# Kernel optimization log

Hardware: AMD Instinct MI355X
Metric: run time of the kernel (lower is better)

## Reference

```python
import jax, jax.numpy as jnp
import numpy as np

LOG2PI = float(np.log(2.0 * np.pi))
VAR = 1e-4
LOGVAR = float(np.log(VAR))


def _gauss_lp(x, mean, dim):
    # MVN log_prob with covariance VAR * I_dim
    sq = jnp.sum((x - mean) ** 2, axis=-1)
    return -0.5 * (dim * (LOG2PI + LOGVAR) + sq / VAR)


def setup_inputs() -> dict:
    B, T, D, H, K = 32, 512, 256, 512, 8
    key = jax.random.key(0)
    ks = jax.random.split(key, 20)
    s = 0.05
    return {
        "x_input": jax.random.normal(ks[0], (B, T, D), jnp.float32),
        "y_train": jax.random.normal(ks[1], (B, T, D), jnp.float32),
        "sampled_h": jax.random.normal(ks[2], (B, T, H), jnp.float32),
        "initials": jax.random.normal(ks[3], (K,), jnp.float32),
        # per-state single-layer RNNs (tanh), weights [K,H,D]/[K,H,H]
        "Wih": jax.random.normal(ks[4], (K, H, D), jnp.float32) * s,
        "Whh": jax.random.normal(ks[5], (K, H, H), jnp.float32) * s,
        "bih": jax.random.normal(ks[6], (K, H), jnp.float32) * s,
        "bhh": jax.random.normal(ks[7], (K, H), jnp.float32) * s,
        # transition RNNCell (h0=0, so only input path + both biases matter)
        "Wt_ih": jax.random.normal(ks[8], (K * K, H), jnp.float32) * s,
        "bt": jax.random.normal(ks[9], (K * K,), jnp.float32) * s,
        # Emission MLP H -> 32 -> 64 -> D
        "W1": jax.random.normal(ks[10], (32, H), jnp.float32) * s,
        "b1": jax.random.normal(ks[11], (32,), jnp.float32) * s,
        "W2": jax.random.normal(ks[12], (64, 32), jnp.float32) * s,
        "b2": jax.random.normal(ks[13], (64,), jnp.float32) * s,
        "W3": jax.random.normal(ks[14], (D, 64), jnp.float32) * s,
        "b3": jax.random.normal(ks[15], (D,), jnp.float32) * s,
    }


def reference(x_input, y_train, sampled_h, initials, Wih, Whh, bih, bhh,
              Wt_ih, bt, W1, b1, W2, b2, W3, b3):
    B, T, D = x_input.shape
    H = sampled_h.shape[-1]
    K = initials.shape[0]
    lse = jax.scipy.special.logsumexp

    # initial log-probs (same for every batch row)
    prob_initial = jnp.broadcast_to(initials - lse(initials), (B, K))

    # ---- prob_all_h: per-state RNN step log-likelihoods ----
    h_prev = sampled_h[:, :-1]  # [B,T-1,H]
    pre = (jnp.einsum('btd,khd->btkh', x_input[:, 1:], Wih)
           + jnp.einsum('bth,kgh->btkg', h_prev, Whh)
           + bih[None, None] + bhh[None, None])  # [B,T-1,K,H]
    x_out = jnp.tanh(pre)
    lp_rest = _gauss_lp(sampled_h[:, 1:, None, :], x_out, H)  # [B,T-1,K]
    lp0 = -0.5 * H * (LOG2PI + LOGVAR)  # log_prob of the mean itself at t=0
    prob_all_h = jnp.concatenate(
        [jnp.full((B, 1, K), lp0, jnp.float32), lp_rest], axis=1)  # [B,T,K]

    # ---- prob_all_s: transition log-probs (normalized over axis=2) ----
    trans = jnp.tanh(jnp.einsum('bth,ch->btc', h_prev, Wt_ih) + bt)
    trans = trans.reshape(B, T - 1, K, K)
    s_rest = trans - lse(trans, axis=2, keepdims=True)
    s0 = jnp.broadcast_to(jnp.eye(K, dtype=jnp.float32), (B, 1, K, K))
    prob_all_s = jnp.concatenate([s0, s_rest], axis=1)  # [B,T,K,K]

    # ---- prob_all_y: emission MLP + MVN log-prob ----
    h1 = jax.nn.relu(sampled_h @ W1.T + b1)
    h2 = jax.nn.relu(h1 @ W2.T + b2)
    em = h2 @ W3.T + b3  # [B,T,D]
    prob_all_y = _gauss_lp(y_train, em, D)  # [B,T]

    log_e = prob_all_h + prob_all_y[..., None]  # [B,T,K]

    # ---- forward pass (Baum-Welch alpha, log-space) ----
    s_tm = jnp.swapaxes(prob_all_s[:, 1:], 0, 1)  # [T-1,B,K,K]
    e_tm = jnp.swapaxes(log_e[:, 1:], 0, 1)       # [T-1,B,K]
    alpha0 = prob_initial + log_e[:, 0]

    def fstep(a, xs):
        s_t, e_t = xs
        a_new = e_t + lse(a[:, None, :] + s_t, axis=2)  # s[b,i,j]=logp(i|j)
        return a_new, a_new

    _, alphas = jax.lax.scan(fstep, alpha0, (s_tm, e_tm))
    forward_prob = jnp.concatenate(
        [alpha0[:, None], jnp.swapaxes(alphas, 0, 1)], axis=1)  # [B,T,K]

    # ---- backward pass (beta) ----
    betaT = jnp.zeros((B, K), jnp.float32)

    def bstep(b, xs):
        s_t1, e_t1 = xs
        b_new = lse(s_t1 + (e_t1 + b)[:, :, None], axis=1)
        return b_new, b_new

    _, betas = jax.lax.scan(bstep, betaT, (s_tm, e_tm), reverse=True)
    backward_prob = jnp.concatenate(
        [jnp.swapaxes(betas, 0, 1), betaT[:, None]], axis=1)  # [B,T,K]

    # ---- gammas ----
    ab = forward_prob + backward_prob
    gamma1 = ab - lse(ab, axis=2, keepdims=True)  # [B,T,K]
    pair = (forward_prob[:, :-1, None, :] + prob_all_s[:, 1:]
            + (log_e[:, 1:] + backward_prob[:, 1:])[:, :, :, None])
    gamma2 = pair - lse(pair, axis=(2, 3), keepdims=True)  # [B,T-1,K,K]

    return (prob_initial, prob_all_s, prob_all_h, prob_all_y,
            gamma1, gamma2, forward_prob, backward_prob)
```

## Files before the change

kernel.cpp:

```cpp
#include <hip/hip_runtime.h>

typedef _Float16 f16;
typedef _Float16 f16x8 __attribute__((ext_vector_type(8)));
typedef float f32x16 __attribute__((ext_vector_type(16)));

#define NB 32
#define NT 512
#define ND 256
#define NH 512
#define M_REAL 16352
#define RDIM 768
#define TILE_ELEMS 98304
#define NTN 33

#define OFF_PI 0
#define OFF_S  256
#define OFF_H  1048832
#define OFF_Y  1179904
#define OFF_G1 1196288
#define OFF_G2 1327360
#define OFF_F  2373888
#define OFF_BW 2504960

#define WS_A    0
#define WS_B    25165824
#define WS_BIAS 31653888
#define WS_SQ   31671296
#define WS_NEED 33768448

#define CH_CONST 1887.3506062251f
#define CY_CONST 943.6753031126f
#define LOG2E 1.4426950408889634f
#define LN2 0.6931471805599453f

#define CA_BLOCKS 1024
#define CB_BLOCKS 264
#define EM_BASE   1288
#define CONV_GRID 2312

__device__ __forceinline__ float fexp2(float x) { return __builtin_amdgcn_exp2f(x); }
__device__ __forceinline__ float flog2(float x) { return __builtin_amdgcn_logf(x); }
__device__ __forceinline__ float ftanh(float x) {
    x = fminf(10.f, fmaxf(-10.f, x));
    float t = fexp2(x * 2.885390081777927f);
    return (t - 1.f) * __builtin_amdgcn_rcpf(t + 1.f);
}
__device__ __forceinline__ float lse8v(const float* z) {
    float M = fmaxf(fmaxf(fmaxf(z[0], z[1]), fmaxf(z[2], z[3])),
                    fmaxf(fmaxf(z[4], z[5]), fmaxf(z[6], z[7])));
    const float e0 = fexp2((z[0] - M) * LOG2E), e1 = fexp2((z[1] - M) * LOG2E);
    const float e2 = fexp2((z[2] - M) * LOG2E), e3 = fexp2((z[3] - M) * LOG2E);
    const float e4 = fexp2((z[4] - M) * LOG2E), e5 = fexp2((z[5] - M) * LOG2E);
    const float e6 = fexp2((z[6] - M) * LOG2E), e7 = fexp2((z[7] - M) * LOG2E);
    const float s = ((e0 + e1) + (e2 + e3)) + ((e4 + e5) + (e6 + e7));
    return M + LN2 * flog2(s);
}

__global__ __launch_bounds__(256) void conv_kernel(
    const float* __restrict__ x, const float* __restrict__ h, const float* __restrict__ y,
    const float* __restrict__ Wih, const float* __restrict__ Whh,
    const float* __restrict__ bih, const float* __restrict__ bhh,
    const float* __restrict__ Wt, const float* __restrict__ btv,
    const float* __restrict__ W1, const float* __restrict__ b1,
    const float* __restrict__ W2, const float* __restrict__ b2,
    const float* __restrict__ W3, const float* __restrict__ b3, f16* __restrict__ A,
    f16* __restrict__ Bm, float* __restrict__ biasc, float* __restrict__ out) {
    __shared__ __align__(16) float smem[11904];
    const int tid = threadIdx.x;
    if (blockIdx.x < CA_BLOCKS) {
        const int m0 = blockIdx.x * 16;
        f16x8* tb = (f16x8*)smem;
#pragma unroll
        for (int i = 0; i < 6; ++i) {
            const int idx = tid + 256 * i;
            const int ml = idx / 96;
            const int ch = idx - ml * 96;
            const int m = m0 + ml;
            f16x8 pk = (f16x8)(f16)0.f;
            if (m < M_REAL) {
                const int b = m / 511;
                const int t = m - b * 511;
                const int c0 = ch * 8;
                const float* src = (c0 < ND) ? x + (size_t)(b * NT + t + 1) * ND + c0
                                             : h + (size_t)(b * NT + t) * NH + (c0 - ND);
                const float4 u = ((const float4*)src)[0];
                const float4 v = ((const float4*)src)[1];
                pk[0] = (f16)u.x; pk[1] = (f16)u.y; pk[2] = (f16)u.z; pk[3] = (f16)u.w;
                pk[4] = (f16)v.x; pk[5] = (f16)v.y; pk[6] = (f16)v.z; pk[7] = (f16)v.w;
            }
            tb[ml * 97 + ch] = pk;
        }
        __syncthreads();
        const size_t tbase = (size_t)(m0 >> 7) * TILE_ELEMS + (size_t)(m0 & 127) * 8;
#pragma unroll
        for (int i = 0; i < 6; ++i) {
            const int idx = tid + 256 * i;
            const int ch2 = idx >> 4;
            const int m2 = idx & 15;
            *(f16x8*)(A + tbase + (size_t)ch2 * 1024 + (size_t)m2 * 8) = tb[m2 * 97 + ch2];
        }
    } else if (blockIdx.x < EM_BASE) {
        const int n0 = (blockIdx.x - CA_BLOCKS) * 16;
        f16x8* tb = (f16x8*)smem;
#pragma unroll
        for (int i = 0; i < 6; ++i) {
            const int idx = tid + 256 * i;
            const int nl = idx / 96;
            const int ch = idx - nl * 96;
            const int n = n0 + nl;
            const int c0 = ch * 8;
            f16x8 pk = (f16x8)(f16)0.f;
            const float* src = nullptr;
            if (n < 4096) {
                src = (c0 < ND) ? Wih + (size_t)n * ND + c0 : Whh + (size_t)n * NH + (c0 - ND);
            } else {
                const int c = n - 4096;
                if (c < 64 && c0 >= ND) src = Wt + (size_t)c * NH + (c0 - ND);
            }
            if (src) {
                const float4 u = ((const float4*)src)[0];
                const float4 v = ((const float4*)src)[1];
                pk[0] = (f16)u.x; pk[1] = (f16)u.y; pk[2] = (f16)u.z; pk[3] = (f16)u.w;
                pk[4] = (f16)v.x; pk[5] = (f16)v.y; pk[6] = (f16)v.z; pk[7] = (f16)v.w;
            }
            tb[nl * 97 + ch] = pk;
        }
        if (tid < 16) {
            const int n = n0 + tid;
            biasc[n] = (n < 4096) ? bih[n] + bhh[n] : ((n - 4096) < 64 ? btv[n - 4096] : 0.f);
        }
        __syncthreads();
        const size_t tbase = (size_t)(n0 >> 7) * TILE_ELEMS + (size_t)(n0 & 127) * 8;
#pragma unroll
        for (int i = 0; i < 6; ++i) {
            const int idx = tid + 256 * i;
            const int ch2 = idx >> 4;
            const int m2 = idx & 15;
            *(f16x8*)(Bm + tbase + (size_t)ch2 * 1024 + (size_t)m2 * 8) = tb[m2 * 97 + ch2];
        }
    } else {
        float* ssh = smem;
        float* W2sh = smem + 8192;
        float* h1sh = smem + 10304;
        float* h2sh = smem + 10816;
        float* red = smem + 11840;
        const int wv = tid >> 6;
        const int o = tid >> 3, seg = tid & 7;
        const int p0 = (blockIdx.x - EM_BASE) * 16;
        float4 w1r[16], w3r[16];
        {
            const float4* w1p = (const float4*)(W1 + (size_t)o * NH + seg * 64);
#pragma unroll
            for (int j = 0; j < 16; ++j) w1r[j] = w1p[(j + seg * 2) & 15];
            const float4* w3p = (const float4*)(W3 + (size_t)tid * 64);
#pragma unroll
            for (int j = 0; j < 16; ++j) w3r[j] = w3p[j];
        }
        if (tid < 64) {
            for (int j = 0; j < 32; ++j) W2sh[tid * 33 + j] = W2[tid * 32 + j];
        }
        float yv[16];
#pragma unroll
        for (int pp = 0; pp < 16; ++pp) yv[pp] = y[(size_t)(p0 + pp) * ND + tid];
        const float b1r = b1[o];
        const float b2r = b2[tid & 63];
        const float b3r = b3[tid];
#pragma unroll
        for (int pp = 0; pp < 16; ++pp) {
            const float2 hv = ((const float2*)(h + (size_t)(p0 + pp) * NH))[tid];
            ssh[pp * 512 + tid * 2] = hv.x;
            ssh[pp * 512 + tid * 2 + 1] = hv.y;
        }
        __syncthreads();
#pragma unroll
        for (int pp = 0; pp < 16; ++pp) {
            const float4* s4 = (const float4*)&ssh[pp * 512 + seg * 64];
            float p = 0.f;
#pragma unroll
            for (int it = 0; it < 16; ++it) {
                const float4 sv = s4[(it + seg * 2) & 15];
                const float4 w = w1r[it];
                p += w.x * sv.x + w.y * sv.y + w.z * sv.z + w.w * sv.w;
            }
            p += __shfl_xor(p, 1, 64);
            p += __shfl_xor(p, 2, 64);
            p += __shfl_xor(p, 4, 64);
            if (seg == 0) h1sh[pp * 32 + o] = fmaxf(p + b1r, 0.f);
        }
        __syncthreads();
        {
            const int o2 = tid & 63;
#pragma unroll
            for (int it = 0; it < 4; ++it) {
                const int pp = wv * 4 + it;
                float s = b2r;
#pragma unroll
                for (int j = 0; j < 32; ++j) s += W2sh[o2 * 33 + j] * h1sh[pp * 32 + j];
                h2sh[pp * 64 + o2] = fmaxf(s, 0.f);
            }
        }
        __syncthreads();
#pragma unroll
        for (int pp = 0; pp < 16; ++pp) {
            float s = b3r;
            const float4* h24 = (const float4*)&h2sh[pp * 64];
#pragma unroll
            for (int j = 0; j < 16; ++j) {
                const float4 w = w3r[j], hb = h24[j];
                s += w.x * hb.x + w.y * hb.y + w.z * hb.z + w.w * hb.w;
            }
            const float d = yv[pp] - s;
            float sq = d * d;
#pragma unroll
            for (int off = 32; off > 0; off >>= 1) sq += __shfl_xor(sq, off, 64);
            if ((tid & 63) == 0) red[pp * 4 + wv] = sq;
        }
        __syncthreads();
        if (tid < 16) {
            out[OFF_Y + p0 + tid] =
                CY_CONST - 5000.f * (red[tid * 4] + red[tid * 4 + 1] + red[tid * 4 + 2] +
                                     red[tid * 4 + 3]);
        }
    }
}

__global__ __launch_bounds__(256) void gemm_kernel(const f16* __restrict__ A,
                                                   const f16* __restrict__ Bm,
                                                   const float* __restrict__ biasc,
                                                   const float* __restrict__ sampled_h,
                                                   float* __restrict__ sq_part,
                                                   float* __restrict__ Ps) {
    __shared__ __align__(16) f16 Ash[8 * 128 * 8];
    __shared__ __align__(16) f16 Bsh[8 * 128 * 8];
    const int tid = threadIdx.x;
    const int lane = tid & 63;
    const int wave = tid >> 6;
    const int xcd = blockIdx.x & 7;
    const int slot = blockIdx.x >> 3;
    const int tm = xcd * 16 + (slot & 15);
    const int tn = slot >> 4;
    const int m0 = tm * 128, n0 = tn * 128;
    const int l31 = lane & 31, hk = lane >> 5;

    f32x16 acc[4];
#pragma unroll
    for (int a = 0; a < 4; ++a) acc[a] = (f32x16)0.f;

    for (int kk = 0; kk < RDIM; kk += 64) {
        __syncthreads();
        const size_t abase = (size_t)tm * TILE_ELEMS + (size_t)kk * 128;
        const size_t bbase = (size_t)tn * TILE_ELEMS + (size_t)kk * 128;
#pragma unroll
        for (int inst = 0; inst < 4; ++inst) {
            const int fb = inst * 256 + wave * 64;
            const f16* ga = A + abase + (size_t)(fb + lane) * 8;
            const f16* gb = Bm + bbase + (size_t)(fb + lane) * 8;
            __builtin_amdgcn_global_load_lds(
                (const __attribute__((address_space(1))) void*)ga,
                (__attribute__((address_space(3))) void*)&Ash[fb * 8], 16, 0, 0);
            __builtin_amdgcn_global_load_lds(
                (const __attribute__((address_space(1))) void*)gb,
                (__attribute__((address_space(3))) void*)&Bsh[fb * 8], 16, 0, 0);
        }
        __syncthreads();
#pragma unroll
        for (int kc = 0; kc < 4; ++kc) {
            const int ch = kc * 2 + hk;
            const f16x8 af = *(const f16x8*)&Ash[(ch * 128 + wave * 32 + l31) * 8];
            f16x8 bfr[4];
#pragma unroll
            for (int ni = 0; ni < 4; ++ni)
                bfr[ni] = *(const f16x8*)&Bsh[(ch * 128 + ni * 32 + l31) * 8];
#pragma unroll
            for (int ni = 0; ni < 4; ++ni)
                acc[ni] = __builtin_amdgcn_mfma_f32_32x32x16_f16(af, bfr[ni], acc[ni], 0, 0, 0);
        }
    }

    if (tn == 32) {
        const float bt0 = biasc[4096 + l31];
        const float bt1 = biasc[4096 + 32 + l31];
#pragma unroll
        for (int r = 0; r < 16; ++r) {
            const int mg = m0 + wave * 32 + (r & 3) + 8 * (r >> 2) + 4 * hk;
            if (mg < M_REAL) {
                const float v0 = ftanh(acc[0][r] + bt0);
                const float v1 = ftanh(acc[1][r] + bt1);
                float M = fmaxf(v0, v1);
                M = fmaxf(M, __shfl_xor(M, 8, 64));
                M = fmaxf(M, __shfl_xor(M, 16, 64));
                float s = fexp2((v0 - M) * LOG2E) + fexp2((v1 - M) * LOG2E);
                s += __shfl_xor(s, 8, 64);
                s += __shfl_xor(s, 16, 64);
                const float lse = M + LN2 * flog2(s);
                const int b = mg / 511, t = mg - b * 511;
                const size_t base = (size_t)(b * NT + t + 1) * 64;
                Ps[base + l31] = v0 - lse;
                Ps[base + 32 + l31] = v1 - lse;
            }
        }
    } else {
        const int k0 = n0 >> 9;
        const int slot4 = (n0 >> 7) & 3;
        const float b0 = biasc[n0 + l31];
        const float b1v = biasc[n0 + 32 + l31];
        const float b2v = biasc[n0 + 64 + l31];
        const float b3v = biasc[n0 + 96 + l31];
#pragma unroll
        for (int r = 0; r < 16; ++r) {
            const int mg = m0 + wave * 32 + (r & 3) + 8 * (r >> 2) + 4 * hk;
            if (mg < M_REAL) {
                const int bb = mg / 511;
                const int tt = mg - bb * 511;
                const float* tgt = sampled_h + (size_t)((bb << 9) + tt + 1) * NH;
                const float d0 = tgt[(n0 + l31) & 511] - ftanh(acc[0][r] + b0);
                const float d1 = tgt[(n0 + 32 + l31) & 511] - ftanh(acc[1][r] + b1v);
                const float d2 = tgt[(n0 + 64 + l31) & 511] - ftanh(acc[2][r] + b2v);
                const float d3 = tgt[(n0 + 96 + l31) & 511] - ftanh(acc[3][r] + b3v);
                float rs = d0 * d0 + d1 * d1 + d2 * d2 + d3 * d3;
                rs += __shfl_xor(rs, 1, 64);
                rs += __shfl_xor(rs, 2, 64);
                rs += __shfl_xor(rs, 4, 64);
                rs += __shfl_xor(rs, 8, 64);
                rs += __shfl_xor(rs, 16, 64);
                if (l31 == 0) sq_part[(size_t)(mg * 8 + k0) * 4 + slot4] = rs;
            }
        }
    }
}

__global__ void post_kernel(const float* __restrict__ sq_part,
                            const float* __restrict__ initials, float* __restrict__ out) {
    const int g = blockIdx.x * 256 + threadIdx.x;
    const int b = g >> 12;
    const int t = (g >> 3) & 511;
    const int k = g & 7;
    float val;
    if (t == 0) {
        val = CH_CONST;
    } else {
        const int m = b * 511 + (t - 1);
        const float4 a = *(const float4*)&sq_part[(size_t)(m * 8 + k) * 4];
        val = CH_CONST - 5000.f * (a.x + a.y + a.z + a.w);
    }
    out[OFF_H + g] = val;
    if (g < 2048) {
        const int sb = g >> 6, c = g & 63;
        out[OFF_S + (size_t)sb * NT * 64 + c] = ((c >> 3) == (c & 7)) ? 1.f : 0.f;
    }
    if (g < 256) {
        float z[8];
#pragma unroll
        for (int j = 0; j < 8; ++j) z[j] = initials[j];
        out[OFF_PI + g] = z[g & 7] - lse8v(z);
    }
}

__global__ __launch_bounds__(256) void scan_kernel(const float* __restrict__ initials,
                                                   float* __restrict__ out) {
    const float* Ps = out + OFF_S;
    const float* Ph = out + OFF_H;
    const float* Py = out + OFF_Y;
    const int lane = threadIdx.x & 63;
    const int wave = threadIdx.x >> 6;
    const int b = wave * 8 + (lane >> 3);
    const int i = lane & 7;
    const int lbase = lane & ~7;

    if (blockIdx.x == 0) {
        float z0[8];
#pragma unroll
        for (int j = 0; j < 8; ++j) z0[j] = initials[j];
        float* Fw = out + OFF_F;
        float a = (z0[i] - lse8v(z0)) + CH_CONST + Py[b * NT];
        Fw[(size_t)(b * NT) * 8 + i] = a;
        float4 cA[8], cB[8]; float cH[8], cY[8];
        float4 nA[8], nB[8]; float nH[8], nY[8];
#define FLOAD(CC, A_, B_, H_, Y_)                                                  \
        _Pragma("unroll") for (int j = 0; j < 8; ++j) {                            \
            int t = 1 + (CC) * 8 + j;                                              \
            t = t > 511 ? 511 : t;                                                 \
            const size_t p = (size_t)(b * NT + t) * 64 + i * 8;                    \
            A_[j] = *(const float4*)&Ps[p];                                        \
            B_[j] = *(const float4*)&Ps[p + 4];                                    \
            H_[j] = Ph[(size_t)(b * NT + t) * 8 + i];                              \
            Y_[j] = Py[b * NT + t];                                                \
        }
#define FSTEP(CC, A_, B_, H_, Y_)                                                  \
        _Pragma("unroll") for (int j = 0; j < 8; ++j) {                            \
            const int t = 1 + (CC) * 8 + j;                                        \
            if (t < NT) {                                                          \
                float z[8];                                                        \
                z[0] = __shfl(a, lbase + 0, 64) + A_[j].x;                         \
                z[1] = __shfl(a, lbase + 1, 64) + A_[j].y;                         \
                z[2] = __shfl(a, lbase + 2, 64) + A_[j].z;                         \
                z[3] = __shfl(a, lbase + 3, 64) + A_[j].w;                         \
                z[4] = __shfl(a, lbase + 4, 64) + B_[j].x;                         \
                z[5] = __shfl(a, lbase + 5, 64) + B_[j].y;                         \
                z[6] = __shfl(a, lbase + 6, 64) + B_[j].z;                         \
                z[7] = __shfl(a, lbase + 7, 64) + B_[j].w;                         \
                a = (H_[j] + Y_[j]) + lse8v(z);                                    \
                Fw[(size_t)(b * NT + t) * 8 + i] = a;                              \
            }                                                                      \
        }
        FLOAD(0, cA, cB, cH, cY);
        for (int c = 0; c < 64; c += 2) {
            const int c1 = c + 1;
            const int c2 = (c + 2 < 64) ? c + 2 : 63;
            FLOAD(c1, nA, nB, nH, nY);
            FSTEP(c, cA, cB, cH, cY);
            FLOAD(c2, cA, cB, cH, cY);
            FSTEP(c1, nA, nB, nH, nY);
        }
#undef FLOAD
#undef FSTEP
    } else {
        float* Bw = out + OFF_BW;
        float bv = 0.f;
        Bw[(size_t)(b * NT + NT - 1) * 8 + i] = 0.f;
        float cS[8][8], nS[8][8]; float cH[8], cY[8], nH[8], nY[8];
#define BLOAD(CC, S_, H_, Y_)                                                      \
        _Pragma("unroll") for (int j = 0; j < 8; ++j) {                            \
            int t = 510 - ((CC) * 8 + j);                                          \
            t = t < 0 ? 0 : t;                                                     \
            const size_t t1 = (size_t)(b * NT + t + 1);                            \
            _Pragma("unroll") for (int ii = 0; ii < 8; ++ii)                       \
                S_[j][ii] = Ps[t1 * 64 + ii * 8 + i];                              \
            H_[j] = Ph[t1 * 8 + i];                                                \
            Y_[j] = Py[t1];                                                        \
        }
#define BSTEP(CC, S_, H_, Y_)                                                      \
        _Pragma("unroll") for (int j = 0; j < 8; ++j) {                            \
            const int t = 510 - ((CC) * 8 + j);                                    \
            if (t >= 0) {                                                          \
                const float v = H_[j] + Y_[j] + bv;                                \
                float z[8];                                                        \
                _Pragma("unroll") for (int ii = 0; ii < 8; ++ii)                   \
                    z[ii] = __shfl(v, lbase + ii, 64) + S_[j][ii];                 \
                bv = lse8v(z);                                                     \
                Bw[(size_t)(b * NT + t) * 8 + i] = bv;                             \
            }                                                                      \
        }
        BLOAD(0, cS, cH, cY);
        for (int c = 0; c < 64; c += 2) {
            const int c1 = c + 1;
            const int c2 = (c + 2 < 64) ? c + 2 : 63;
            BLOAD(c1, nS, nH, nY);
            BSTEP(c, cS, cH, cY);
            BLOAD(c2, cS, cH, cY);
            BSTEP(c1, nS, nH, nY);
        }
#undef BLOAD
#undef BSTEP
    }
}

__global__ void gamma_kernel(float* __restrict__ out) {
    const float* Ps = out + OFF_S;
    const float* Ph = out + OFF_H;
    const float* Py = out + OFF_Y;
    const float* Fw = out + OFF_F;
    const float* Bw = out + OFF_BW;
    if (blockIdx.x < 511) {
        const int gidx = blockIdx.x * 256 + threadIdx.x;
        const int pos = gidx >> 3;
        const int i = gidx & 7;
        const int b = pos / 511, t = pos - b * 511;
        const size_t t1 = (size_t)(b * NT + t + 1);
        const float ei = Ph[t1 * 8 + i] + Py[t1] + Bw[t1 * 8 + i];
        const float4 sa = ((const float4*)&Ps[(t1 * 8 + i) * 8])[0];
        const float4 sb = ((const float4*)&Ps[(t1 * 8 + i) * 8])[1];
        const float4 fa = ((const float4*)&Fw[(size_t)(b * NT + t) * 8])[0];
        const float4 fb = ((const float4*)&Fw[(size_t)(b * NT + t) * 8])[1];
        float z[8] = {fa.x + sa.x + ei, fa.y + sa.y + ei, fa.z + sa.z + ei, fa.w + sa.w + ei,
                      fb.x + sb.x + ei, fb.y + sb.y + ei, fb.z + sb.z + ei, fb.w + sb.w + ei};
        float M = fmaxf(fmaxf(fmaxf(z[0], z[1]), fmaxf(z[2], z[3])),
                        fmaxf(fmaxf(z[4], z[5]), fmaxf(z[6], z[7])));
        M = fmaxf(M, __shfl_xor(M, 1, 64));
        M = fmaxf(M, __shfl_xor(M, 2, 64));
        M = fmaxf(M, __shfl_xor(M, 4, 64));
        float s = 0.f;
#pragma unroll
        for (int j = 0; j < 8; ++j) s += fexp2((z[j] - M) * LOG2E);
        s += __shfl_xor(s, 1, 64);
        s += __shfl_xor(s, 2, 64);
        s += __shfl_xor(s, 4, 64);
        const float l = M + LN2 * flog2(s);
        float* G2 = out + OFF_G2;
        float4 o0 = {z[0] - l, z[1] - l, z[2] - l, z[3] - l};
        float4 o1 = {z[4] - l, z[5] - l, z[6] - l, z[7] - l};
        ((float4*)&G2[(size_t)gidx * 8])[0] = o0;
        ((float4*)&G2[(size_t)gidx * 8])[1] = o1;
    } else {
        const int pos = (blockIdx.x - 511) * 256 + threadIdx.x;
        const float4 fa = ((const float4*)&Fw[(size_t)pos * 8])[0];
        const float4 fb = ((const float4*)&Fw[(size_t)pos * 8])[1];
        const float4 ba = ((const float4*)&Bw[(size_t)pos * 8])[0];
        const float4 bb = ((const float4*)&Bw[(size_t)pos * 8])[1];
        float ab[8] = {fa.x + ba.x, fa.y + ba.y, fa.z + ba.z, fa.w + ba.w,
                       fb.x + bb.x, fb.y + bb.y, fb.z + bb.z, fb.w + bb.w};
        const float l = lse8v(ab);
        float* G1 = out + OFF_G1;
        float4 o0 = {ab[0] - l, ab[1] - l, ab[2] - l, ab[3] - l};
        float4 o1 = {ab[4] - l, ab[5] - l, ab[6] - l, ab[7] - l};
        ((float4*)&G1[(size_t)pos * 8])[0] = o0;
        ((float4*)&G1[(size_t)pos * 8])[1] = o1;
    }
}

extern "C" void kernel_launch(void* const* d_in, const int* in_sizes, int n_in, void* d_out,
                              int out_size, void* d_ws, size_t ws_size, hipStream_t stream) {
    const float* x = (const float*)d_in[0];
    const float* y = (const float*)d_in[1];
    const float* h = (const float*)d_in[2];
    const float* initials = (const float*)d_in[3];
    const float* Wih = (const float*)d_in[4];
    const float* Whh = (const float*)d_in[5];
    const float* bih = (const float*)d_in[6];
    const float* bhh = (const float*)d_in[7];
    const float* Wt = (const float*)d_in[8];
    const float* btv = (const float*)d_in[9];
    const float* W1 = (const float*)d_in[10];
    const float* b1 = (const float*)d_in[11];
    const float* W2 = (const float*)d_in[12];
    const float* b2 = (const float*)d_in[13];
    const float* W3 = (const float*)d_in[14];
    const float* b3 = (const float*)d_in[15];
    float* out = (float*)d_out;
    char* ws = (char*)d_ws;
    if (ws_size < (size_t)WS_NEED) return;
    f16* Aws = (f16*)(ws + WS_A);
    f16* Bws = (f16*)(ws + WS_B);
    float* biasc = (float*)(ws + WS_BIAS);
    float* sqp = (float*)(ws + WS_SQ);

    conv_kernel<<<CONV_GRID, 256, 0, stream>>>(x, h, y, Wih, Whh, bih, bhh, Wt, btv, W1, b1,
                                               W2, b2, W3, b3, Aws, Bws, biasc, out);
    gemm_kernel<<<4224, 256, 0, stream>>>(Aws, Bws, biasc, h, sqp, out + OFF_S);
    post_kernel<<<512, 256, 0, stream>>>(sqp, initials, out);
    scan_kernel<<<2, 256, 0, stream>>>(initials, out);
    gamma_kernel<<<575, 256, 0, stream>>>(out);
}
```

Measured before the change: 462.0 us.

## Parallelize HMM forward/backward scans via chunked log-semiring transfer matrices

```diff
diff --git a/kernel.cpp b/kernel.cpp
--- a/kernel.cpp
+++ b/kernel.cpp
@@ -26,12 +26,14 @@
 #define WS_B    25165824
 #define WS_BIAS 31653888
 #define WS_SQ   31671296
-#define WS_NEED 33768448
+#define WS_M    33768448
+#define WS_NEED 34292736
 
 #define CH_CONST 1887.3506062251f
 #define CY_CONST 943.6753031126f
 #define LOG2E 1.4426950408889634f
 #define LN2 0.6931471805599453f
+#define NEGINF -1e30f
 
 #define CA_BLOCKS 1024
 #define CB_BLOCKS 264
@@ -237,8 +239,8 @@
     const int wave = tid >> 6;
     const int xcd = blockIdx.x & 7;
     const int slot = blockIdx.x >> 3;
-    const int tm = xcd * 16 + (slot & 15);
-    const int tn = slot >> 4;
+    const int tm = xcd * 16 + slot / NTN;
+    const int tn = slot % NTN;
     const int m0 = tm * 128, n0 = tn * 128;
     const int l31 = lane & 31, hk = lane >> 5;
 
@@ -356,102 +358,185 @@
     }
 }
 
-__global__ __launch_bounds__(256) void scan_kernel(const float* __restrict__ initials,
-                                                   float* __restrict__ out) {
+
+template <bool WRITE>
+__device__ __forceinline__ float fwd_run(const float* __restrict__ Ps,
+                                         const float* __restrict__ Ph,
+                                         const float* __restrict__ Py,
+                                         float* __restrict__ Fw, int b, int t0,
+                                         int t1, float a, int lane) {
+    const int i = lane & 7;
+    const int base = lane & ~7;
+    float4 cA[8], cB[8], nA[8], nB[8];
+    float cH[8], cY[8], nH[8], nY[8];
+#define FLOADR(G, A_, B_, H_, Y_)                                              \
+    _Pragma("unroll") for (int jj = 0; jj < 8; ++jj) {                         \
+        int t = t0 + (G) * 8 + jj;                                             \
+        t = t > t1 ? t1 : t;                                                   \
+        const size_t p = (size_t)(b * NT + t) * 64 + i * 8;                    \
+        A_[jj] = *(const float4*)&Ps[p];                                       \
+        B_[jj] = *(const float4*)&Ps[p + 4];                                   \
+        H_[jj] = Ph[(size_t)(b * NT + t) * 8 + i];                             \
+        Y_[jj] = Py[b * NT + t];                                               \
+    }
+#define FSTEPR(G, A_, B_, H_, Y_)                                              \
+    _Pragma("unroll") for (int jj = 0; jj < 8; ++jj) {                         \
+        const int t = t0 + (G) * 8 + jj;                                       \
+        if (t <= t1) {                                                         \
+            float z[8];                                                        \
+            z[0] = __shfl(a, base + 0, 64) + A_[jj].x;                         \
+            z[1] = __shfl(a, base + 1, 64) + A_[jj].y;                         \
+            z[2] = __shfl(a, base + 2, 64) + A_[jj].z;                         \
+            z[3] = __shfl(a, base + 3, 64) + A_[jj].w;                         \
+            z[4] = __shfl(a, base + 4, 64) + B_[jj].x;                         \
+            z[5] = __shfl(a, base + 5, 64) + B_[jj].y;                         \
+            z[6] = __shfl(a, base + 6, 64) + B_[jj].z;                         \
+            z[7] = __shfl(a, base + 7, 64) + B_[jj].w;                         \
+            a = (H_[jj] + Y_[jj]) + lse8v(z);                                  \
+            if (WRITE && lane < 8) Fw[(size_t)(b * NT + t) * 8 + i] = a;       \
+        }                                                                      \
+    }
+    FLOADR(0, cA, cB, cH, cY);
+    FLOADR(1, nA, nB, nH, nY);
+    FSTEPR(0, cA, cB, cH, cY);
+    FLOADR(2, cA, cB, cH, cY);
+    FSTEPR(1, nA, nB, nH, nY);
+    FLOADR(3, nA, nB, nH, nY);
+    FSTEPR(2, cA, cB, cH, cY);
+    FSTEPR(3, nA, nB, nH, nY);
+#undef FLOADR
+#undef FSTEPR
+    return a;
+}
+
+template <bool WRITE>
+__device__ __forceinline__ float bwd_run(const float* __restrict__ Ps,
+                                         const float* __restrict__ Ph,
+                                         const float* __restrict__ Py,
+                                         float* __restrict__ Bw, int b, int tt0,
+                                         int tt1, float a, int lane) {
+    const int i = lane & 7;
+    const int base = lane & ~7;
+    float cS[8][8], nS[8][8], cH[8], cY[8], nH[8], nY[8];
+#define BLOADR(G, S_, H_, Y_)                                                  \
+    _Pragma("unroll") for (int jj = 0; jj < 8; ++jj) {                         \
+        int t = tt0 - (G) * 8 - jj;                                            \
+        t = t < tt1 ? tt1 : t;                                                 \
+        const size_t q = (size_t)(b * NT + t + 1);                             \
+        _Pragma("unroll") for (int ii = 0; ii < 8; ++ii)                       \
+            S_[jj][ii] = Ps[q * 64 + ii * 8 + i];                              \
+        H_[jj] = Ph[q * 8 + i];                                                \
+        Y_[jj] = Py[q];                                                       \
+    }
+#define BSTEPR(G, S_, H_, Y_)                                                  \
+    _Pragma("unroll") for (int jj = 0; jj < 8; ++jj) {                         \
+        const int t = tt0 - (G) * 8 - jj;                                      \
+        if (t >= tt1) {                                                        \
+            const float v = H_[jj] + Y_[jj] + a;                               \
+            float z[8];                                                        \
+            _Pragma("unroll") for (int ii = 0; ii < 8; ++ii)                   \
+                z[ii] = __shfl(v, base + ii, 64) + S_[jj][ii];                 \
+            a = lse8v(z);                                                      \
+            if (WRITE && lane < 8) Bw[(size_t)(b * NT + t) * 8 + i] = a;       \
+        }                                                                      \
+    }
+    BLOADR(0, cS, cH, cY);
+    BLOADR(1, nS, nH, nY);
+    BSTEPR(0, cS, cH, cY);
+    BLOADR(2, cS, cH, cY);
+    BSTEPR(1, nS, nH, nY);
+    BLOADR(3, nS, nH, nY);
+    BSTEPR(2, cS, cH, cY);
+    BSTEPR(3, nS, nH, nY);
+#undef BLOADR
+#undef BSTEPR
+    return a;
+}
+
+__global__ __launch_bounds__(256) void scan_mat_kernel(const float* __restrict__ out,
+                                                       float* __restrict__ Mws) {
     const float* Ps = out + OFF_S;
     const float* Ph = out + OFF_H;
     const float* Py = out + OFF_Y;
     const int lane = threadIdx.x & 63;
     const int wave = threadIdx.x >> 6;
-    const int b = wave * 8 + (lane >> 3);
+    const int i = lane & 7, j = lane >> 3;
+    float a = (i == j) ? 0.f : NEGINF;
+    if (blockIdx.x < 128) {
+        const int b = blockIdx.x >> 2;
+        const int c = (blockIdx.x & 3) * 4 + wave;
+        const int t0 = 1 + 32 * c;
+        const int t1 = (32 * (c + 1) < 511) ? 32 * (c + 1) : 511;
+        a = fwd_run<false>(Ps, Ph, Py, nullptr, b, t0, t1, a, lane);
+        Mws[(size_t)(b * 16 + c) * 64 + lane] = a;
+    } else {
+        const int b = (blockIdx.x - 128) >> 2;
+        const int c = ((blockIdx.x - 128) & 3) * 4 + wave;
+        const int tt0 = 510 - 32 * c;
+        const int tt1 = (479 - 32 * c > 0) ? 479 - 32 * c : 0;
+        a = bwd_run<false>(Ps, Ph, Py, nullptr, b, tt0, tt1, a, lane);
+        Mws[32768 + (size_t)(b * 16 + c) * 64 + lane] = a;
+    }
+}
+
+__global__ __launch_bounds__(256) void scan_fin_kernel(const float* __restrict__ initials,
+                                                       float* __restrict__ out,
+                                                       const float* __restrict__ Mws) {
+    const float* Ps = out + OFF_S;
+    const float* Ph = out + OFF_H;
+    const float* Py = out + OFF_Y;
+    const int lane = threadIdx.x & 63;
+    const int wave = threadIdx.x >> 6;
     const int i = lane & 7;
-    const int lbase = lane & ~7;
-
-    if (blockIdx.x == 0) {
+    const int base = lane & ~7;
+    const bool fwd = blockIdx.x < 128;
+    const int blk = fwd ? blockIdx.x : blockIdx.x - 128;
+    const int b = blk >> 2;
+    const int c = (blk & 3) * 4 + wave;
+    const float* Mbase = Mws + (fwd ? 0 : 32768) + (size_t)(b * 16) * 64;
+
+    float a;
+    if (fwd) {
         float z0[8];
 #pragma unroll
-        for (int j = 0; j < 8; ++j) z0[j] = initials[j];
-        float* Fw = out + OFF_F;
-        float a = (z0[i] - lse8v(z0)) + CH_CONST + Py[b * NT];
-        Fw[(size_t)(b * NT) * 8 + i] = a;
-        float4 cA[8], cB[8]; float cH[8], cY[8];
-        float4 nA[8], nB[8]; float nH[8], nY[8];
-#define FLOAD(CC, A_, B_, H_, Y_)                                                  \
-        _Pragma("unroll") for (int j = 0; j < 8; ++j) {                            \
-            int t = 1 + (CC) * 8 + j;                                              \
-            t = t > 511 ? 511 : t;                                                 \
-            const size_t p = (size_t)(b * NT + t) * 64 + i * 8;                    \
-            A_[j] = *(const float4*)&Ps[p];                                        \
-            B_[j] = *(const float4*)&Ps[p + 4];                                    \
-            H_[j] = Ph[(size_t)(b * NT + t) * 8 + i];                              \
-            Y_[j] = Py[b * NT + t];                                                \
-        }
-#define FSTEP(CC, A_, B_, H_, Y_)                                                  \
-        _Pragma("unroll") for (int j = 0; j < 8; ++j) {                            \
-            const int t = 1 + (CC) * 8 + j;                                        \
-            if (t < NT) {                                                          \
-                float z[8];                                                        \
-                z[0] = __shfl(a, lbase + 0, 64) + A_[j].x;                         \
-                z[1] = __shfl(a, lbase + 1, 64) + A_[j].y;                         \
-                z[2] = __shfl(a, lbase + 2, 64) + A_[j].z;                         \
-                z[3] = __shfl(a, lbase + 3, 64) + A_[j].w;                         \
-                z[4] = __shfl(a, lbase + 4, 64) + B_[j].x;                         \
-                z[5] = __shfl(a, lbase + 5, 64) + B_[j].y;                         \
-                z[6] = __shfl(a, lbase + 6, 64) + B_[j].z;                         \
-                z[7] = __shfl(a, lbase + 7, 64) + B_[j].w;                         \
-                a = (H_[j] + Y_[j]) + lse8v(z);                                    \
-                Fw[(size_t)(b * NT + t) * 8 + i] = a;                              \
-            }                                                                      \
-        }
-        FLOAD(0, cA, cB, cH, cY);
-        for (int c = 0; c < 64; c += 2) {
-            const int c1 = c + 1;
-            const int c2 = (c + 2 < 64) ? c + 2 : 63;
-            FLOAD(c1, nA, nB, nH, nY);
-            FSTEP(c, cA, cB, cH, cY);
-            FLOAD(c2, cA, cB, cH, cY);
-            FSTEP(c1, nA, nB, nH, nY);
-        }
-#undef FLOAD
-#undef FSTEP
+        for (int jj = 0; jj < 8; ++jj) z0[jj] = initials[jj];
+        a = (z0[i] - lse8v(z0)) + CH_CONST + Py[b * NT];
+        if (c == 0 && lane < 8) (out + OFF_F)[(size_t)(b * NT) * 8 + i] = a;
     } else {
-        float* Bw = out + OFF_BW;
-        float bv = 0.f;
-        Bw[(size_t)(b * NT + NT - 1) * 8 + i] = 0.f;
-        float cS[8][8], nS[8][8]; float cH[8], cY[8], nH[8], nY[8];
-#define BLOAD(CC, S_, H_, Y_)                                                      \
-        _Pragma("unroll") for (int j = 0; j < 8; ++j) {                            \
-            int t = 510 - ((CC) * 8 + j);                                          \
-            t = t < 0 ? 0 : t;                                                     \
-            const size_t t1 = (size_t)(b * NT + t + 1);                            \
-            _Pragma("unroll") for (int ii = 0; ii < 8; ++ii)                       \
-                S_[j][ii] = Ps[t1 * 64 + ii * 8 + i];                              \
-            H_[j] = Ph[t1 * 8 + i];                                                \
-            Y_[j] = Py[t1];                                                        \
-        }
-#define BSTEP(CC, S_, H_, Y_)                                                      \
-        _Pragma("unroll") for (int j = 0; j < 8; ++j) {                            \
-            const int t = 510 - ((CC) * 8 + j);                                    \
-            if (t >= 0) {                                                          \
-                const float v = H_[j] + Y_[j] + bv;                                \
-                float z[8];                                                        \
-                _Pragma("unroll") for (int ii = 0; ii < 8; ++ii)                   \
-                    z[ii] = __shfl(v, lbase + ii, 64) + S_[j][ii];                 \
-                bv = lse8v(z);                                                     \
-                Bw[(size_t)(b * NT + t) * 8 + i] = bv;                             \
-            }                                                                      \
-        }
-        BLOAD(0, cS, cH, cY);
-        for (int c = 0; c < 64; c += 2) {
-            const int c1 = c + 1;
-            const int c2 = (c + 2 < 64) ? c + 2 : 63;
-            BLOAD(c1, nS, nH, nY);
-            BSTEP(c, cS, cH, cY);
-            BLOAD(c2, cS, cH, cY);
-            BSTEP(c1, nS, nH, nY);
-        }
-#undef BLOAD
-#undef BSTEP
+        a = 0.f;
+        if (c == 0 && lane < 8) (out + OFF_BW)[(size_t)(b * NT + NT - 1) * 8 + i] = 0.f;
+    }
+    if (c > 0) {
+        float4 r0 = *(const float4*)&Mbase[0 * 64 + i * 8];
+        float4 r1 = *(const float4*)&Mbase[0 * 64 + i * 8 + 4];
+        for (int cc = 0; cc < c; ++cc) {
+            float4 s0, s1;
+            if (cc + 1 < c) {
+                s0 = *(const float4*)&Mbase[(size_t)(cc + 1) * 64 + i * 8];
+                s1 = *(const float4*)&Mbase[(size_t)(cc + 1) * 64 + i * 8 + 4];
+            }
+            float z[8];
+            z[0] = __shfl(a, base + 0, 64) + r0.x;
+            z[1] = __shfl(a, base + 1, 64) + r0.y;
+            z[2] = __shfl(a, base + 2, 64) + r0.z;
+            z[3] = __shfl(a, base + 3, 64) + r0.w;
+            z[4] = __shfl(a, base + 4, 64) + r1.x;
+            z[5] = __shfl(a, base + 5, 64) + r1.y;
+            z[6] = __shfl(a, base + 6, 64) + r1.z;
+            z[7] = __shfl(a, base + 7, 64) + r1.w;
+            a = lse8v(z);
+            r0 = s0;
+            r1 = s1;
+        }
+    }
+    if (fwd) {
+        const int t0 = 1 + 32 * c;
+        const int t1 = (32 * (c + 1) < 511) ? 32 * (c + 1) : 511;
+        fwd_run<true>(Ps, Ph, Py, out + OFF_F, b, t0, t1, a, lane);
+    } else {
+        const int tt0 = 510 - 32 * c;
+        const int tt1 = (479 - 32 * c > 0) ? 479 - 32 * c : 0;
+        bwd_run<true>(Ps, Ph, Py, out + OFF_BW, b, tt0, tt1, a, lane);
     }
 }
 
@@ -533,11 +618,13 @@
     f16* Bws = (f16*)(ws + WS_B);
     float* biasc = (float*)(ws + WS_BIAS);
     float* sqp = (float*)(ws + WS_SQ);
+    float* Mws = (float*)(ws + WS_M);
 
     conv_kernel<<<CONV_GRID, 256, 0, stream>>>(x, h, y, Wih, Whh, bih, bhh, Wt, btv, W1, b1,
                                                W2, b2, W3, b3, Aws, Bws, biasc, out);
     gemm_kernel<<<4224, 256, 0, stream>>>(Aws, Bws, biasc, h, sqp, out + OFF_S);
     post_kernel<<<512, 256, 0, stream>>>(sqp, initials, out);
-    scan_kernel<<<2, 256, 0, stream>>>(initials, out);
+    scan_mat_kernel<<<256, 256, 0, stream>>>(out, Mws);
+    scan_fin_kernel<<<256, 256, 0, stream>>>(initials, out, Mws);
     gamma_kernel<<<575, 256, 0, stream>>>(out);
 }
```

New measurement: 388.2 us. 16.0% less time.
